# Performance work log

Hardware: AMD Instinct MI355X
Metric: run time of the kernel (lower is better)

The kernel has to match this reference:

```python
import jax, jax.numpy as jnp
import numpy as np

SEQ, B, IN, H = 512, 64, 256, 512

def _lin_params(key, out_d, in_d):
    k1, k2 = jax.random.split(key)
    bound = 1.0 / np.sqrt(in_d)
    w = jax.random.uniform(k1, (out_d, in_d), jnp.float32, -bound, bound)
    b = jax.random.uniform(k2, (out_d,), jnp.float32, -bound, bound)
    return w, b

def setup_inputs() -> dict:
    key = jax.random.key(0)
    ks = jax.random.split(key, 9)
    x = jax.random.normal(ks[0], (SEQ, B, IN), jnp.float32)
    h0 = jnp.zeros((B, H), jnp.float32)
    c0 = jnp.zeros((B, H), jnp.float32)
    Wf_w, Wf_b = _lin_params(ks[1], H, IN)
    Uf_w, Uf_b = _lin_params(ks[2], H, H)
    Wi_w, Wi_b = _lin_params(ks[3], H, IN)
    Ui_w, Ui_b = _lin_params(ks[4], H, H)
    Wo_w, Wo_b = _lin_params(ks[5], H, IN)
    Uo_w, Uo_b = _lin_params(ks[6], H, H)
    Wc_w, Wc_b = _lin_params(ks[7], H, IN)
    Uc_w, Uc_b = _lin_params(ks[8], H, H)
    return dict(x=x, h0=h0, c0=c0,
                Wf_w=Wf_w, Wf_b=Wf_b, Uf_w=Uf_w, Uf_b=Uf_b,
                Wi_w=Wi_w, Wi_b=Wi_b, Ui_w=Ui_w, Ui_b=Ui_b,
                Wo_w=Wo_w, Wo_b=Wo_b, Uo_w=Uo_w, Uo_b=Uo_b,
                Wc_w=Wc_w, Wc_b=Wc_b, Uc_w=Uc_w, Uc_b=Uc_b)

def reference(x, h0, c0,
              Wf_w, Wf_b, Uf_w, Uf_b,
              Wi_w, Wi_b, Ui_w, Ui_b,
              Wo_w, Wo_b, Uo_w, Uo_b,
              Wc_w, Wc_b, Uc_w, Uc_b):
    # Precompute all input-to-hidden projections in one batched GEMM per gate.
    xf = jnp.einsum('tbi,hi->tbh', x, Wf_w) + Wf_b  # (T,B,H)
    xi = jnp.einsum('tbi,hi->tbh', x, Wi_w) + Wi_b
    xo = jnp.einsum('tbi,hi->tbh', x, Wo_w) + Wo_b
    xc = jnp.einsum('tbi,hi->tbh', x, Wc_w) + Wc_b

    def step(carry, xs):
        h, c = carry
        xft, xit, xot, xct = xs
        f = jax.nn.sigmoid(xft + h @ Uf_w.T + Uf_b)
        i = jax.nn.sigmoid(xit + h @ Ui_w.T + Ui_b)
        o = jax.nn.sigmoid(xot + h @ Uo_w.T + Uo_b)
        c = f * c + i * jnp.tanh(xct + h @ Uc_w.T + Uc_b)
        h = o * jnp.tanh(c)
        return (h, c), h

    (h, c), h_seq = jax.lax.scan(step, (h0, c0), (xf, xi, xo, xc))
    return h_seq, h, c
```

## Files before the change

kernel.cpp:

```cpp
#include <hip/hip_runtime.h>


#define T_STEPS 512
#define BATCH   64
#define IN_D    256
#define HID     512
#define NGROUP  4
#define NSLICE  16
#define BLK_B   16
#define BLK_H   32
#define THREADS 512
#define ROW_BYTES  1024
#define GRP_BYTES  (BLK_B * ROW_BYTES)
#define SLOT_BYTES (NGROUP * GRP_BYTES)
#define FLAGS_OFF  (2 * SLOT_BYTES)
#define NFLAGS     (NGROUP * NSLICE)

using short8  = __attribute__((ext_vector_type(8))) short;
using int4v   = __attribute__((ext_vector_type(4))) int;
using float4v = __attribute__((ext_vector_type(4))) float;

#define FRAG_ADDR(f) (((f) << 4) + (((f) >> 4) << 4))

__device__ __forceinline__ unsigned short f2bf(float f) {
    union { float f; unsigned int i; } v; v.f = f;
    unsigned int r = v.i + 0x7fff + ((v.i >> 16) & 1);
    return (unsigned short)(r >> 16);
}
__device__ __forceinline__ short8 pack8(float4 a, float4 b) {
    short8 s;
    s[0]=(short)f2bf(a.x); s[1]=(short)f2bf(a.y); s[2]=(short)f2bf(a.z); s[3]=(short)f2bf(a.w);
    s[4]=(short)f2bf(b.x); s[5]=(short)f2bf(b.y); s[6]=(short)f2bf(b.z); s[7]=(short)f2bf(b.w);
    return s;
}
__device__ __forceinline__ float sigm(float v) { return 1.0f / (1.0f + __expf(-v)); }
__device__ __forceinline__ float tanh_(float v) { return 2.0f / (1.0f + __expf(-2.0f * v)) - 1.0f; }

__device__ __forceinline__ void lds_barrier() {
    asm volatile("s_waitcnt lgkmcnt(0)" ::: "memory");
    __builtin_amdgcn_s_barrier();
    __builtin_amdgcn_sched_barrier(0);
}

__global__ __launch_bounds__(256, 1) void lstm_init_ws(unsigned int* w, int n) {
    int i = blockIdx.x * blockDim.x + threadIdx.x;
    if (i < n) __hip_atomic_store(&w[i], 0u, __ATOMIC_RELAXED, __HIP_MEMORY_SCOPE_AGENT);
}

__global__ __launch_bounds__(THREADS, 1) void lstm_persist(
    const float* __restrict__ x,
    const float* __restrict__ h0,
    const float* __restrict__ c0,
    const float* __restrict__ Wf, const float* __restrict__ Wfb,
    const float* __restrict__ Uf, const float* __restrict__ Ufb,
    const float* __restrict__ Wi, const float* __restrict__ Wib,
    const float* __restrict__ Ui, const float* __restrict__ Uib,
    const float* __restrict__ Wo, const float* __restrict__ Wob,
    const float* __restrict__ Uo, const float* __restrict__ Uob,
    const float* __restrict__ Wc, const float* __restrict__ Wcb,
    const float* __restrict__ Uc, const float* __restrict__ Ucb,
    float* out,
    unsigned char* exch)
{
    __shared__ __attribute__((aligned(16))) unsigned char hfrag[17392];
    __shared__ __attribute__((aligned(16))) unsigned char xfrag[8688];
    __shared__ float g_lds[8 * 256];

    const int tid  = threadIdx.x;
    const int lane = tid & 63;
    const int wave = tid >> 6;
    const int gate = wave >> 1;
    const int hlf  = wave & 1;
    const int grp  = blockIdx.x & 3;
    const int slc  = blockIdx.x >> 2;
    const int bb   = grp * BLK_B;
    const int hbase= slc * BLK_H;
    const int lm   = lane & 15;
    const int lq   = lane >> 4;
    const int row  = tid >> 5;
    const int seg  = tid & 31;

    const float* Ug  = (gate == 0) ? Uf : (gate == 1) ? Ui : (gate == 2) ? Uo : Uc;
    const float* Wg  = (gate == 0) ? Wf : (gate == 1) ? Wi : (gate == 2) ? Wo : Wc;
    const float* Wbg = (gate == 0) ? Wfb : (gate == 1) ? Wib : (gate == 2) ? Wob : Wcb;
    const float* Ubg = (gate == 0) ? Ufb : (gate == 1) ? Uib : (gate == 2) ? Uob : Ucb;
    const int ng = hbase + hlf * 16 + lm;

    short8 ufrag[16];
#pragma unroll
    for (int ks = 0; ks < 16; ++ks) {
        const float* p = Ug + (size_t)ng * HID + ks * 32 + lq * 8;
        ufrag[ks] = pack8(*(const float4*)(p), *(const float4*)(p + 4));
    }
    short8 wfrag[8];
#pragma unroll
    for (int ks = 0; ks < 8; ++ks) {
        const float* p = Wg + (size_t)ng * IN_D + ks * 32 + lq * 8;
        wfrag[ks] = pack8(*(const float4*)(p), *(const float4*)(p + 4));
    }
    const float bias = Wbg[ng] + Ubg[ng];

    float c_reg = c0[(size_t)(bb + row) * HID + hbase + seg];

    {
        const float* ph = h0 + (size_t)(bb + row) * HID + seg * 16;
        int f0 = (seg >> 1) * 64 + (seg & 1) * 32 + row;
        *(short8*)(hfrag + FRAG_ADDR(f0))      = pack8(*(const float4*)(ph),     *(const float4*)(ph + 4));
        *(short8*)(hfrag + FRAG_ADDR(f0 + 16)) = pack8(*(const float4*)(ph + 8), *(const float4*)(ph + 12));

        const float* px = x + (size_t)(bb + row) * IN_D + seg * 8;
        int fx = (seg >> 2) * 64 + (seg & 3) * 16 + row;
        *(short8*)(xfrag + FRAG_ADDR(fx)) = pack8(*(const float4*)(px), *(const float4*)(px + 4));
    }
    float4 xa0, xa1, xb0 = {0,0,0,0}, xb1 = {0,0,0,0};
    {
        const float* px = x + ((size_t)1 * BATCH + bb + row) * IN_D + seg * 8;
        xa0 = *(const float4*)(px); xa1 = *(const float4*)(px + 4);
    }
    __syncthreads();

    float4v accx0 = {bias, bias, bias, bias};
    float4v accx1 = {0.f, 0.f, 0.f, 0.f};
#pragma unroll
    for (int ks = 0; ks < 8; ++ks) {
        short8 a = *(const short8*)(xfrag + FRAG_ADDR(ks * 64 + lane));
        if (ks & 1) accx1 = __builtin_amdgcn_mfma_f32_16x16x32_bf16(a, wfrag[ks], accx1, 0, 0, 0);
        else        accx0 = __builtin_amdgcn_mfma_f32_16x16x32_bf16(a, wfrag[ks], accx0, 0, 0, 0);
    }

    float* const out_h = out + (size_t)T_STEPS * BATCH * HID;
    float* const out_c = out_h + (size_t)BATCH * HID;

    unsigned char* const ex_wr = exch + (size_t)grp * GRP_BYTES
                               + (size_t)row * ROW_BYTES + (size_t)(hbase + seg) * 2;
    const unsigned char* const ex_rd = exch + (size_t)grp * GRP_BYTES + (size_t)tid * 32;
    unsigned int* const flg = (unsigned int*)(exch + FLAGS_OFF) + grp * NSLICE;
    unsigned int* const flg_wr = flg + slc;

    auto STEP = [&](int t, float4& sx0, float4& sx1, float4& px0, float4& px1) {
        float4v acc0 = accx0, acc1 = accx1;
#pragma unroll
        for (int ks = 0; ks < 16; ++ks) {
            short8 a = *(const short8*)(hfrag + FRAG_ADDR(ks * 64 + lane));
            if (ks & 1) acc1 = __builtin_amdgcn_mfma_f32_16x16x32_bf16(a, ufrag[ks], acc1, 0, 0, 0);
            else        acc0 = __builtin_amdgcn_mfma_f32_16x16x32_bf16(a, ufrag[ks], acc0, 0, 0, 0);
        }
        float4v acc = acc0 + acc1;
#pragma unroll
        for (int r = 0; r < 4; ++r)
            g_lds[wave * 256 + (lq * 4 + r) * 16 + lm] = acc[r];

        if (t + 1 < T_STEPS) {
            int fx = (seg >> 2) * 64 + (seg & 3) * 16 + row;
            *(short8*)(xfrag + FRAG_ADDR(fx)) = pack8(sx0, sx1);
        }

        lds_barrier();

        float hv;
        {
            int hf2 = seg >> 4, nn = seg & 15;
            float fpre = g_lds[(0 * 2 + hf2) * 256 + row * 16 + nn];
            float ipre = g_lds[(1 * 2 + hf2) * 256 + row * 16 + nn];
            float opre = g_lds[(2 * 2 + hf2) * 256 + row * 16 + nn];
            float gpre = g_lds[(3 * 2 + hf2) * 256 + row * 16 + nn];
            float fv = sigm(fpre), iv = sigm(ipre), ov = sigm(opre);
            float gv = tanh_(gpre);
            c_reg = fv * c_reg + iv * gv;
            hv = ov * tanh_(c_reg);
        }
        out[((size_t)t * BATCH + bb + row) * HID + hbase + seg] = hv;

        if (t + 1 < T_STEPS) {
            {
                unsigned int bfv = f2bf(hv);
                unsigned int nb  = (unsigned int)__shfl_xor((int)bfv, 1);
                if ((tid & 1) == 0) {
                    unsigned int pw = bfv | (nb << 16);
                    const unsigned char* pa = ex_wr + (size_t)(t & 1) * SLOT_BYTES;
                    asm volatile("global_store_dword %0, %1, off sc0 sc1"
                                 :: "v"(pa), "v"(pw) : "memory");
                }
            }
            asm volatile("s_waitcnt vmcnt(0)" ::: "memory");
            __builtin_amdgcn_s_barrier();
            __builtin_amdgcn_sched_barrier(0);
            if (tid == 0) {
                asm volatile("global_store_dword %0, %1, off sc0 sc1"
                             :: "v"(flg_wr), "v"((unsigned int)(t + 1)) : "memory");
            }

            {
                int tn = (t + 2 < T_STEPS) ? (t + 2) : (T_STEPS - 1);
                const float* px = x + ((size_t)tn * BATCH + bb + row) * IN_D + seg * 8;
                px0 = *(const float4*)(px); px1 = *(const float4*)(px + 4);
            }

            accx0 = (float4v){bias, bias, bias, bias};
            accx1 = (float4v){0.f, 0.f, 0.f, 0.f};
#pragma unroll
            for (int ks = 0; ks < 8; ++ks) {
                short8 a = *(const short8*)(xfrag + FRAG_ADDR(ks * 64 + lane));
                if (ks & 1) accx1 = __builtin_amdgcn_mfma_f32_16x16x32_bf16(a, wfrag[ks], accx1, 0, 0, 0);
                else        accx0 = __builtin_amdgcn_mfma_f32_16x16x32_bf16(a, wfrag[ks], accx0, 0, 0, 0);
            }

            if (tid == 0) {
                const unsigned int want = (unsigned int)(t + 1);
                int4v q0, q1, q2, q3;
                long guard = 0;
                for (;;) {
                    asm volatile(
                        "global_load_dwordx4 %0, %4, off sc0 sc1\n\t"
                        "global_load_dwordx4 %1, %4, off offset:16 sc0 sc1\n\t"
                        "global_load_dwordx4 %2, %4, off offset:32 sc0 sc1\n\t"
                        "global_load_dwordx4 %3, %4, off offset:48 sc0 sc1\n\t"
                        "s_waitcnt vmcnt(0)"
                        : "=&v"(q0), "=&v"(q1), "=&v"(q2), "=&v"(q3)
                        : "v"(flg) : "memory");
                    bool ok = true;
#pragma unroll
                    for (int j = 0; j < 4; ++j) {
                        ok &= ((unsigned int)q0[j] >= want);
                        ok &= ((unsigned int)q1[j] >= want);
                        ok &= ((unsigned int)q2[j] >= want);
                        ok &= ((unsigned int)q3[j] >= want);
                    }
                    if (ok) break;
                    if (++guard > (1L << 22)) break;
                }
            }
            __builtin_amdgcn_s_barrier();
            __builtin_amdgcn_sched_barrier(0);

            {
                const unsigned char* pb = ex_rd + (size_t)(t & 1) * SLOT_BYTES;
                int4v e0, e1;
                asm volatile(
                    "global_load_dwordx4 %0, %2, off sc0 sc1\n\t"
                    "global_load_dwordx4 %1, %2, off offset:16 sc0 sc1\n\t"
                    "s_waitcnt vmcnt(0)"
                    : "=&v"(e0), "=&v"(e1) : "v"(pb) : "memory");
                int f0 = (seg >> 1) * 64 + (seg & 1) * 32 + row;
                *(int4v*)(hfrag + FRAG_ADDR(f0))      = e0;
                *(int4v*)(hfrag + FRAG_ADDR(f0 + 16)) = e1;
            }
            lds_barrier();
        } else {
            out_h[(size_t)(bb + row) * HID + hbase + seg] = hv;
            out_c[(size_t)(bb + row) * HID + hbase + seg] = c_reg;
        }
    };

    for (int t = 0; t < T_STEPS; t += 2) {
        STEP(t,     xa0, xa1, xb0, xb1);
        STEP(t + 1, xb0, xb1, xa0, xa1);
    }
}

extern "C" void kernel_launch(void* const* d_in, const int* in_sizes, int n_in,
                              void* d_out, int out_size, void* d_ws, size_t ws_size,
                              hipStream_t stream) {
    (void)in_sizes; (void)n_in; (void)out_size; (void)ws_size;
    const float* x   = (const float*)d_in[0];
    const float* h0  = (const float*)d_in[1];
    const float* c0  = (const float*)d_in[2];
    const float* Wf  = (const float*)d_in[3];
    const float* Wfb = (const float*)d_in[4];
    const float* Uf  = (const float*)d_in[5];
    const float* Ufb = (const float*)d_in[6];
    const float* Wi  = (const float*)d_in[7];
    const float* Wib = (const float*)d_in[8];
    const float* Ui  = (const float*)d_in[9];
    const float* Uib = (const float*)d_in[10];
    const float* Wo  = (const float*)d_in[11];
    const float* Wob = (const float*)d_in[12];
    const float* Uo  = (const float*)d_in[13];
    const float* Uob = (const float*)d_in[14];
    const float* Wc  = (const float*)d_in[15];
    const float* Wcb = (const float*)d_in[16];
    const float* Uc  = (const float*)d_in[17];
    const float* Ucb = (const float*)d_in[18];

    unsigned char* exch = (unsigned char*)d_ws;
    unsigned int* flags = (unsigned int*)(exch + FLAGS_OFF);
    lstm_init_ws<<<1, 256, 0, stream>>>(flags, NFLAGS);
    lstm_persist<<<NGROUP * NSLICE, THREADS, 0, stream>>>(
        x, h0, c0,
        Wf, Wfb, Uf, Ufb, Wi, Wib, Ui, Uib,
        Wo, Wob, Uo, Uob, Wc, Wcb, Uc, Ucb,
        (float*)d_out, exch);
}
```

Before: 1.532 ms.

## Embed step tags in exchange chunks to replace separate flag barrier

Each hidden-state chunk written to the global exchange buffer now carries the step number next to its data. Writers no longer wait for their stores to drain and then publish a separate flag. A sentinel poll by one thread checks that the group's chunks have arrived, and each thread then spins on its own chunk's tags before copying the data into LDS. The input-projection MFMAs and the output store are moved so they overlap the exchange latency, and the gate LDS buffer is padded to avoid bank conflicts. The risks are weaker ordering guarantees between the data and the tag within a single 16-byte store, a larger exchange buffer that must be zeroed, and more polling traffic.

```diff
diff --git a/kernel.cpp b/kernel.cpp
--- a/kernel.cpp
+++ b/kernel.cpp
@@ -10,11 +10,8 @@
 #define BLK_B   16
 #define BLK_H   32
 #define THREADS 512
-#define ROW_BYTES  1024
-#define GRP_BYTES  (BLK_B * ROW_BYTES)
-#define SLOT_BYTES (NGROUP * GRP_BYTES)
-#define FLAGS_OFF  (2 * SLOT_BYTES)
-#define NFLAGS     (NGROUP * NSLICE)
+#define CH_ROW  128
+#define SLOT_BYTES (BATCH * CH_ROW * 16)
 
 using short8  = __attribute__((ext_vector_type(8))) short;
 using int4v   = __attribute__((ext_vector_type(4))) int;
@@ -64,7 +61,7 @@
 {
     __shared__ __attribute__((aligned(16))) unsigned char hfrag[17392];
     __shared__ __attribute__((aligned(16))) unsigned char xfrag[8688];
-    __shared__ float g_lds[8 * 256];
+    __shared__ float g_lds[8 * 320];
 
     const int tid  = threadIdx.x;
     const int lane = tid & 63;
@@ -131,11 +128,11 @@
     float* const out_h = out + (size_t)T_STEPS * BATCH * HID;
     float* const out_c = out_h + (size_t)BATCH * HID;
 
-    unsigned char* const ex_wr = exch + (size_t)grp * GRP_BYTES
-                               + (size_t)row * ROW_BYTES + (size_t)(hbase + seg) * 2;
-    const unsigned char* const ex_rd = exch + (size_t)grp * GRP_BYTES + (size_t)tid * 32;
-    unsigned int* const flg = (unsigned int*)(exch + FLAGS_OFF) + grp * NSLICE;
-    unsigned int* const flg_wr = flg + slc;
+    unsigned char* const ex_wr = exch
+        + (size_t)((bb + row) * CH_ROW + slc * 8 + (seg >> 2)) * 16;
+    const unsigned char* const ex_rd = exch
+        + (size_t)((bb + row) * CH_ROW + seg * 4) * 16;
+    const unsigned char* const snt = exch + (size_t)bb * CH_ROW * 16 + 8;
 
     auto STEP = [&](int t, float4& sx0, float4& sx1, float4& px0, float4& px1) {
         float4v acc0 = accx0, acc1 = accx1;
@@ -148,7 +145,7 @@
         float4v acc = acc0 + acc1;
 #pragma unroll
         for (int r = 0; r < 4; ++r)
-            g_lds[wave * 256 + (lq * 4 + r) * 16 + lm] = acc[r];
+            g_lds[wave * 320 + lq * 80 + r * 16 + lm] = acc[r];
 
         if (t + 1 < T_STEPS) {
             int fx = (seg >> 2) * 64 + (seg & 3) * 16 + row;
@@ -160,35 +157,81 @@
         float hv;
         {
             int hf2 = seg >> 4, nn = seg & 15;
-            float fpre = g_lds[(0 * 2 + hf2) * 256 + row * 16 + nn];
-            float ipre = g_lds[(1 * 2 + hf2) * 256 + row * 16 + nn];
-            float opre = g_lds[(2 * 2 + hf2) * 256 + row * 16 + nn];
-            float gpre = g_lds[(3 * 2 + hf2) * 256 + row * 16 + nn];
+            int rbase = (row >> 2) * 80 + (row & 3) * 16 + nn;
+            float fpre = g_lds[(0 * 2 + hf2) * 320 + rbase];
+            float ipre = g_lds[(1 * 2 + hf2) * 320 + rbase];
+            float opre = g_lds[(2 * 2 + hf2) * 320 + rbase];
+            float gpre = g_lds[(3 * 2 + hf2) * 320 + rbase];
             float fv = sigm(fpre), iv = sigm(ipre), ov = sigm(opre);
             float gv = tanh_(gpre);
             c_reg = fv * c_reg + iv * gv;
             hv = ov * tanh_(c_reg);
         }
-        out[((size_t)t * BATCH + bb + row) * HID + hbase + seg] = hv;
 
         if (t + 1 < T_STEPS) {
+            const size_t so = (size_t)(t & 1) * SLOT_BYTES;
+            const unsigned int want = (unsigned int)(t + 1);
+
             {
                 unsigned int bfv = f2bf(hv);
                 unsigned int nb  = (unsigned int)__shfl_xor((int)bfv, 1);
-                if ((tid & 1) == 0) {
-                    unsigned int pw = bfv | (nb << 16);
-                    const unsigned char* pa = ex_wr + (size_t)(t & 1) * SLOT_BYTES;
-                    asm volatile("global_store_dword %0, %1, off sc0 sc1"
-                                 :: "v"(pa), "v"(pw) : "memory");
+                unsigned int p   = bfv | (nb << 16);
+                unsigned int q   = (unsigned int)__shfl_xor((int)p, 2);
+                if ((tid & 3) == 0) {
+                    int4v ch; ch[0] = (int)p; ch[1] = (int)q;
+                    ch[2] = (int)want; ch[3] = (int)want;
+                    asm volatile("global_store_dwordx4 %0, %1, off sc0 sc1"
+                                 :: "v"(ex_wr + so), "v"(ch) : "memory");
                 }
             }
-            asm volatile("s_waitcnt vmcnt(0)" ::: "memory");
+
+            accx0 = (float4v){bias, bias, bias, bias};
+            accx1 = (float4v){0.f, 0.f, 0.f, 0.f};
+#pragma unroll
+            for (int ks = 0; ks < 8; ++ks) {
+                short8 a = *(const short8*)(xfrag + FRAG_ADDR(ks * 64 + lane));
+                if (ks & 1) accx1 = __builtin_amdgcn_mfma_f32_16x16x32_bf16(a, wfrag[ks], accx1, 0, 0, 0);
+                else        accx0 = __builtin_amdgcn_mfma_f32_16x16x32_bf16(a, wfrag[ks], accx0, 0, 0, 0);
+            }
+
+            if (tid == 2) {
+                const unsigned char* sb = snt + so;
+                unsigned int v0,v1,v2,v3,v4,v5,v6,v7,v8,v9,v10,v11,v12,v13,v14,v15;
+                long guard = 0;
+                for (;;) {
+                    asm volatile(
+                        "global_load_dword %0,  %16, off sc0 sc1\n\t"
+                        "global_load_dword %1,  %16, off offset:128 sc0 sc1\n\t"
+                        "global_load_dword %2,  %16, off offset:256 sc0 sc1\n\t"
+                        "global_load_dword %3,  %16, off offset:384 sc0 sc1\n\t"
+                        "global_load_dword %4,  %16, off offset:512 sc0 sc1\n\t"
+                        "global_load_dword %5,  %16, off offset:640 sc0 sc1\n\t"
+                        "global_load_dword %6,  %16, off offset:768 sc0 sc1\n\t"
+                        "global_load_dword %7,  %16, off offset:896 sc0 sc1\n\t"
+                        "global_load_dword %8,  %16, off offset:1024 sc0 sc1\n\t"
+                        "global_load_dword %9,  %16, off offset:1152 sc0 sc1\n\t"
+                        "global_load_dword %10, %16, off offset:1280 sc0 sc1\n\t"
+                        "global_load_dword %11, %16, off offset:1408 sc0 sc1\n\t"
+                        "global_load_dword %12, %16, off offset:1536 sc0 sc1\n\t"
+                        "global_load_dword %13, %16, off offset:1664 sc0 sc1\n\t"
+                        "global_load_dword %14, %16, off offset:1792 sc0 sc1\n\t"
+                        "global_load_dword %15, %16, off offset:1920 sc0 sc1\n\t"
+                        "s_waitcnt vmcnt(0)"
+                        : "=&v"(v0),"=&v"(v1),"=&v"(v2),"=&v"(v3),
+                          "=&v"(v4),"=&v"(v5),"=&v"(v6),"=&v"(v7),
+                          "=&v"(v8),"=&v"(v9),"=&v"(v10),"=&v"(v11),
+                          "=&v"(v12),"=&v"(v13),"=&v"(v14),"=&v"(v15)
+                        : "v"(sb) : "memory");
+                    bool ok = (v0 >= want) & (v1 >= want) & (v2 >= want) & (v3 >= want)
+                            & (v4 >= want) & (v5 >= want) & (v6 >= want) & (v7 >= want)
+                            & (v8 >= want) & (v9 >= want) & (v10 >= want) & (v11 >= want)
+                            & (v12 >= want) & (v13 >= want) & (v14 >= want) & (v15 >= want);
+                    if (ok) break;
+                    if (++guard > (1L << 22)) break;
+                }
+            }
             __builtin_amdgcn_s_barrier();
             __builtin_amdgcn_sched_barrier(0);
-            if (tid == 0) {
-                asm volatile("global_store_dword %0, %1, off sc0 sc1"
-                             :: "v"(flg_wr), "v"((unsigned int)(t + 1)) : "memory");
-            }
 
             {
                 int tn = (t + 2 < T_STEPS) ? (t + 2) : (T_STEPS - 1);
@@ -196,18 +239,9 @@
                 px0 = *(const float4*)(px); px1 = *(const float4*)(px + 4);
             }
 
-            accx0 = (float4v){bias, bias, bias, bias};
-            accx1 = (float4v){0.f, 0.f, 0.f, 0.f};
-#pragma unroll
-            for (int ks = 0; ks < 8; ++ks) {
-                short8 a = *(const short8*)(xfrag + FRAG_ADDR(ks * 64 + lane));
-                if (ks & 1) accx1 = __builtin_amdgcn_mfma_f32_16x16x32_bf16(a, wfrag[ks], accx1, 0, 0, 0);
-                else        accx0 = __builtin_amdgcn_mfma_f32_16x16x32_bf16(a, wfrag[ks], accx0, 0, 0, 0);
-            }
-
-            if (tid == 0) {
-                const unsigned int want = (unsigned int)(t + 1);
-                int4v q0, q1, q2, q3;
+            {
+                const unsigned char* pb = ex_rd + so;
+                int4v e0, e1, e2, e3;
                 long guard = 0;
                 for (;;) {
                     asm volatile(
@@ -216,37 +250,22 @@
                         "global_load_dwordx4 %2, %4, off offset:32 sc0 sc1\n\t"
                         "global_load_dwordx4 %3, %4, off offset:48 sc0 sc1\n\t"
                         "s_waitcnt vmcnt(0)"
-                        : "=&v"(q0), "=&v"(q1), "=&v"(q2), "=&v"(q3)
-                        : "v"(flg) : "memory");
-                    bool ok = true;
-#pragma unroll
-                    for (int j = 0; j < 4; ++j) {
-                        ok &= ((unsigned int)q0[j] >= want);
-                        ok &= ((unsigned int)q1[j] >= want);
-                        ok &= ((unsigned int)q2[j] >= want);
-                        ok &= ((unsigned int)q3[j] >= want);
-                    }
-                    if (ok) break;
+                        : "=&v"(e0), "=&v"(e1), "=&v"(e2), "=&v"(e3)
+                        : "v"(pb) : "memory");
+                    if (((unsigned int)e0[2] == want) & ((unsigned int)e1[2] == want) &
+                        ((unsigned int)e2[2] == want) & ((unsigned int)e3[2] == want)) break;
                     if (++guard > (1L << 22)) break;
                 }
-            }
-            __builtin_amdgcn_s_barrier();
-            __builtin_amdgcn_sched_barrier(0);
-
-            {
-                const unsigned char* pb = ex_rd + (size_t)(t & 1) * SLOT_BYTES;
-                int4v e0, e1;
-                asm volatile(
-                    "global_load_dwordx4 %0, %2, off sc0 sc1\n\t"
-                    "global_load_dwordx4 %1, %2, off offset:16 sc0 sc1\n\t"
-                    "s_waitcnt vmcnt(0)"
-                    : "=&v"(e0), "=&v"(e1) : "v"(pb) : "memory");
                 int f0 = (seg >> 1) * 64 + (seg & 1) * 32 + row;
-                *(int4v*)(hfrag + FRAG_ADDR(f0))      = e0;
-                *(int4v*)(hfrag + FRAG_ADDR(f0 + 16)) = e1;
-            }
+                *(int4v*)(hfrag + FRAG_ADDR(f0))      = (int4v){e0[0], e0[1], e1[0], e1[1]};
+                *(int4v*)(hfrag + FRAG_ADDR(f0 + 16)) = (int4v){e2[0], e2[1], e3[0], e3[1]};
+            }
+
+            out[((size_t)t * BATCH + bb + row) * HID + hbase + seg] = hv;
+
             lds_barrier();
         } else {
+            out[((size_t)t * BATCH + bb + row) * HID + hbase + seg] = hv;
             out_h[(size_t)(bb + row) * HID + hbase + seg] = hv;
             out_c[(size_t)(bb + row) * HID + hbase + seg] = c_reg;
         }
@@ -283,8 +302,8 @@
     const float* Ucb = (const float*)d_in[18];
 
     unsigned char* exch = (unsigned char*)d_ws;
-    unsigned int* flags = (unsigned int*)(exch + FLAGS_OFF);
-    lstm_init_ws<<<1, 256, 0, stream>>>(flags, NFLAGS);
+    const int nzero = 2 * SLOT_BYTES / 4;
+    lstm_init_ws<<<(nzero + 255) / 256, 256, 0, stream>>>((unsigned int*)exch, nzero);
     lstm_persist<<<NGROUP * NSLICE, THREADS, 0, stream>>>(
         x, h0, c0,
         Wf, Wfb, Uf, Ufb, Wi, Wib, Ui, Uib,
```

Result: slower. 1.636 ms (+6.8%).
